# Kernel tuning notes

Hardware: AMD Instinct MI355X
Metric: run time of the kernel (lower is better)

The kernel has to match this reference:

```python
import jax, jax.numpy as jnp
import numpy as np

HEADS = 8
DIM_HEAD = 64
SCALE = DIM_HEAD ** -0.5


def setup_inputs() -> dict:
    key = jax.random.key(0)
    ks = jax.random.split(key, 5)
    dim, hidden = 512, HEADS * DIM_HEAD
    b, l = 4, 2048
    return {
        "x": jax.random.normal(ks[0], (b, dim, l), jnp.float32),
        "w_qkv": jax.random.normal(ks[1], (3 * hidden, dim), jnp.float32) * 0.02,
        "b_qkv": jax.random.normal(ks[2], (3 * hidden,), jnp.float32) * 0.02,
        "w_out": jax.random.normal(ks[3], (dim, hidden), jnp.float32) * 0.02,
        "b_out": jax.random.normal(ks[4], (dim,), jnp.float32) * 0.02,
    }


def reference(x, w_qkv, b_qkv, w_out, b_out):
    b, c, l = x.shape
    # Conv1d kernel-size-1 == per-position linear: (b, 3*hidden, l)
    qkv = jnp.einsum('oc,bcl->bol', w_qkv, x) + b_qkv[None, :, None]
    q, k, v = jnp.split(qkv, 3, axis=1)
    # rearrange 'b (h d) l -> b h d l'
    def split_heads(t):
        return t.reshape(b, HEADS, DIM_HEAD, l)
    q, k, v = split_heads(q) * SCALE, split_heads(k), split_heads(v)
    sim = jnp.einsum('bhdi,bhdj->bhij', q, k)  # [b,h,l,l]
    sim = sim - jax.lax.stop_gradient(jnp.max(sim, axis=-1, keepdims=True))
    attn = jax.nn.softmax(sim, axis=-1)
    out = jnp.einsum('bhij,bhdj->bhid', attn, v)  # [b,h,l,d]
    # 'b h l d -> b (h d) l'
    out = out.transpose(0, 1, 3, 2).reshape(b, HEADS * DIM_HEAD, l)
    out = jnp.einsum('oc,bcl->bol', w_out, out) + b_out[None, :, None]
    return out
```

## Files before the change

kernel.cpp:

```cpp
#include <hip/hip_runtime.h>
#include <hip/hip_bf16.h>

#define B 4
#define DIM 512
#define HID 512
#define NH 8
#define DH 64
#define L 2048
#define QSCALE (0.125f * 1.4426950408889634f)

typedef __attribute__((ext_vector_type(8)))  short bf16x8;
typedef __attribute__((ext_vector_type(4)))  float f32x4;
typedef __attribute__((ext_vector_type(16))) float f32x16;
typedef __attribute__((ext_vector_type(4)))  int   i32x4;

static __device__ __forceinline__ short f32_to_bf16s(float f) {
    __hip_bfloat16 h = __float2bfloat16(f);
    return *reinterpret_cast<short*>(&h);
}
static __device__ __forceinline__ float bf16s_to_f32(short s) {
    return __uint_as_float(((unsigned)(unsigned short)s) << 16);
}

static __device__ __forceinline__ float fast_exp2(float x) {
    float r;
    asm("v_exp_f32 %0, %1" : "=v"(r) : "v"(x));
    return r;
}

static __device__ __forceinline__ void gl_lds16(const short* g, short* l) {
    __builtin_amdgcn_global_load_lds(
        (const __attribute__((address_space(1))) void*)g,
        (__attribute__((address_space(3))) void*)l, 16, 0, 0);
}

static __device__ __forceinline__ bf16x8 lds_frag(const short* t, int row, int c) {
    bf16x8 v;
    __builtin_memcpy(&v, t + row * 64 + ((c ^ (row & 7)) * 8), 16);
    return v;
}

static __device__ __forceinline__ bf16x8 lds_vfrag(const short* t, int row,
                                                   int c0, int me4) {
    int2 a, b;
    __builtin_memcpy(&a, t + row * 64 + ((c0 ^ (row & 7)) * 8 + me4), 8);
    __builtin_memcpy(&b, t + row * 64 + (((c0 + 1) ^ (row & 7)) * 8 + me4), 8);
    i32x4 v = {a.x, a.y, b.x, b.y};
    return __builtin_bit_cast(bf16x8, v);
}

__global__ __launch_bounds__(256) void prep(
    const float* __restrict__ wq, const float* __restrict__ wo,
    short* __restrict__ wdst,
    const float* __restrict__ X, short* __restrict__ XT)
{
    const int bx  = blockIdx.x;
    const int tid = threadIdx.x;
    if (bx < 1024) {
        const int i = (bx * 256 + tid) * 4;
        float4 v;
        if (i < 786432) v = *(const float4*)(wq + i);
        else            v = *(const float4*)(wo + (i - 786432));
        short4 pk = {f32_to_bf16s(v.x), f32_to_bf16s(v.y),
                     f32_to_bf16s(v.z), f32_to_bf16s(v.w)};
        *(short4*)(wdst + i) = pk;
        return;
    }
    const int bid = bx - 1024;
    const int l0 = (bid & 31) * 64;
    const int c0 = ((bid >> 5) & 7) * 64;
    const int b  = bid >> 8;

    __shared__ float tile[64][65];
    const float* Xb = X + (size_t)b * DIM * L;

    #pragma unroll
    for (int it = 0; it < 16; ++it) {
        const int cr = (tid >> 6) + it * 4;
        const int lc = tid & 63;
        tile[cr][lc] = Xb[(size_t)(c0 + cr) * L + l0 + lc];
    }
    __syncthreads();
    short* XTb = XT + (size_t)b * L * DIM;
    #pragma unroll
    for (int it = 0; it < 8; ++it) {
        const int l  = (tid >> 5) + it * 8;
        const int c2 = (tid & 31) * 2;
        short2 pk = {f32_to_bf16s(tile[c2][l]), f32_to_bf16s(tile[c2 + 1][l])};
        *(short2*)(XTb + (size_t)(l0 + l) * DIM + c0 + c2) = pk;
    }
}

__global__ __launch_bounds__(256) void qkv_mfma(
    const short* __restrict__ Wb, const short* __restrict__ XT,
    const float* __restrict__ bias,
    short* __restrict__ qws, short* __restrict__ kws, short* __restrict__ vws)
{
    const int lBase = blockIdx.x * 128;
    const int oBase = blockIdx.y * 128;
    const int b     = blockIdx.z;
    const int tid   = threadIdx.x;
    const int wave  = tid >> 6;
    const int lane  = tid & 63;
    const int lid   = lane & 15;
    const int quad  = lane >> 4;
    const int rsub  = lane >> 3;
    const int cl    = (lane & 7) ^ rsub;

    __shared__ __align__(16) short Wt[128 * 64];
    __shared__ __align__(16) short Xt[128 * 64];

    const short* XTb = XT + (size_t)b * L * DIM;
    const int oLoc = (wave & 1) * 64;
    const int lLoc = (wave >> 1) * 64;

    f32x4 acc[4][4];
    #pragma unroll
    for (int mi = 0; mi < 4; ++mi)
        #pragma unroll
        for (int ni = 0; ni < 4; ++ni) acc[mi][ni] = (f32x4){0.f, 0.f, 0.f, 0.f};

    for (int c0 = 0; c0 < DIM; c0 += 64) {
        if (c0) __syncthreads();
        #pragma unroll
        for (int t = 0; t < 4; ++t) {
            const int ch = wave * 4 + t;
            const int r  = ch * 8 + rsub;
            gl_lds16(Wb  + (size_t)(oBase + r) * DIM + c0 + cl * 8, Wt + ch * 512);
            gl_lds16(XTb + (size_t)(lBase + r) * DIM + c0 + cl * 8, Xt + ch * 512);
        }
        __syncthreads();
        #pragma unroll
        for (int kc = 0; kc < 2; ++kc) {
            bf16x8 a[4], bb[4];
            #pragma unroll
            for (int mi = 0; mi < 4; ++mi)
                a[mi] = lds_frag(Wt, oLoc + mi * 16 + lid, kc * 4 + quad);
            #pragma unroll
            for (int ni = 0; ni < 4; ++ni)
                bb[ni] = lds_frag(Xt, lLoc + ni * 16 + lid, kc * 4 + quad);
            #pragma unroll
            for (int mi = 0; mi < 4; ++mi)
                #pragma unroll
                for (int ni = 0; ni < 4; ++ni)
                    acc[mi][ni] = __builtin_amdgcn_mfma_f32_16x16x32_bf16(
                        a[mi], bb[ni], acc[mi][ni], 0, 0, 0);
        }
    }

    const int rty = oBase >> 9;
    const float sc = (rty == 0) ? QSCALE : 1.0f;
    const int h = ((oBase + oLoc) >> 6) & 7;

    #pragma unroll
    for (int mi = 0; mi < 4; ++mi) {
        const int dB = mi * 16 + quad * 4;
        float bia[4];
        #pragma unroll
        for (int r = 0; r < 4; ++r)
            bia[r] = bias[oBase + oLoc + mi * 16 + quad * 4 + r];

        if (rty < 2) {
            short* dst = (rty == 0 ? qws : kws) + (((size_t)b * NH + h) * L) * DH;
            #pragma unroll
            for (int ni = 0; ni < 4; ++ni) {
                const int l = lBase + lLoc + ni * 16 + lid;
                short4 pk = {f32_to_bf16s((acc[mi][ni][0] + bia[0]) * sc),
                             f32_to_bf16s((acc[mi][ni][1] + bia[1]) * sc),
                             f32_to_bf16s((acc[mi][ni][2] + bia[2]) * sc),
                             f32_to_bf16s((acc[mi][ni][3] + bia[3]) * sc)};
                *(short4*)(dst + (size_t)l * DH + dB) = pk;
            }
        } else {
            short* dst = vws + (((size_t)b * NH + h) * DH) * L;
            #pragma unroll
            for (int r = 0; r < 4; ++r) {
                const int d = dB + r;
                #pragma unroll
                for (int ni = 0; ni < 4; ++ni)
                    dst[(size_t)d * L + lBase + lLoc + ni * 16 + lid] =
                        f32_to_bf16s((acc[mi][ni][r] + bia[r]) * sc);
            }
        }
    }
}

__global__ __launch_bounds__(256) void attn_mfma(
    const short* __restrict__ Q, const short* __restrict__ K,
    const short* __restrict__ VT,
    short* __restrict__ Op0, short* __restrict__ Op1,
    short* __restrict__ Op2, short* __restrict__ Op3,
    float* __restrict__ Lp)
{
    const int h     = blockIdx.x >> 2;
    const int qtr   = blockIdx.x & 3;
    const int b     = blockIdx.y;
    const int iTile = blockIdx.z;
    const int tid   = threadIdx.x;
    const int wave  = tid >> 6;
    const int lane  = tid & 63;
    const int l5    = lane & 31;
    const int me    = lane >> 5;
    const int me4   = me * 4;
    const int rsub  = lane >> 3;
    const int cl    = (lane & 7) ^ rsub;

    short* __restrict__ Op = (qtr & 2) ? ((qtr & 1) ? Op3 : Op2)
                                       : ((qtr & 1) ? Op1 : Op0);
    float* __restrict__ Lq = Lp + (size_t)qtr * (B * NH * L);

    const size_t headOff = ((size_t)b * NH + h) * (size_t)L * DH;
    const short* Qh = Q + headOff;
    const short* Kh = K + headOff;
    const short* Vh = VT + headOff;

    __shared__ __align__(16) short Kt[64 * 64];
    __shared__ __align__(16) short Vt[64 * 64];

    const int q0 = iTile * 128 + wave * 32;
    bf16x8 qf[4];
    #pragma unroll
    for (int kc = 0; kc < 4; ++kc)
        qf[kc] = *(const bf16x8*)(Qh + (size_t)(q0 + l5) * DH + kc * 16 + me4 * 2);

    const i32x4 onesI = {0x3F803F80, 0x3F803F80, 0x3F803F80, 0x3F803F80};
    const bf16x8 ones = __builtin_bit_cast(bf16x8, onesI);

    f32x16 oacc[2], lacc;
    #pragma unroll
    for (int dt = 0; dt < 2; ++dt)
        #pragma unroll
        for (int r = 0; r < 16; ++r) oacc[dt][r] = 0.f;
    #pragma unroll
    for (int r = 0; r < 16; ++r) lacc[r] = 0.f;

    const int jt0 = qtr * 8;
    for (int it = 0; it < 8; ++it) {
        const int j0 = (jt0 + it) * 64;
        if (it) __syncthreads();
        #pragma unroll
        for (int t = 0; t < 2; ++t) {
            const int ch = wave * 2 + t;
            const int r  = ch * 8 + rsub;
            gl_lds16(Kh + (size_t)(j0 + r) * DH + cl * 8, Kt + ch * 512);
            gl_lds16(Vh + (size_t)r * L + j0 + cl * 8,    Vt + ch * 512);
        }
        __syncthreads();

        unsigned dw[2][4][2];
        #pragma unroll
        for (int mt = 0; mt < 2; ++mt) {
            f32x16 s;
            #pragma unroll
            for (int r = 0; r < 16; ++r) s[r] = 0.f;
            #pragma unroll
            for (int kc = 0; kc < 4; ++kc) {
                bf16x8 a = lds_frag(Kt, mt * 32 + l5, kc * 2 + me);
                s = __builtin_amdgcn_mfma_f32_32x32x16_bf16(a, qf[kc], s, 0, 0, 0);
            }
            #pragma unroll
            for (int g = 0; g < 4; ++g) {
                #pragma unroll
                for (int p = 0; p < 2; ++p) {
                    const float p0 = fast_exp2(s[4 * g + 2 * p]);
                    const float p1 = fast_exp2(s[4 * g + 2 * p + 1]);
                    dw[mt][g][p] = __builtin_amdgcn_perm(
                        __float_as_uint(p1), __float_as_uint(p0), 0x07060302u);
                }
            }
        }

        #pragma unroll
        for (int mt = 0; mt < 2; ++mt) {
            #pragma unroll
            for (int kl = 0; kl < 2; ++kl) {
                i32x4 bi = {(int)dw[mt][2 * kl][0], (int)dw[mt][2 * kl][1],
                            (int)dw[mt][2 * kl + 1][0], (int)dw[mt][2 * kl + 1][1]};
                bf16x8 pb = __builtin_bit_cast(bf16x8, bi);
                lacc = __builtin_amdgcn_mfma_f32_32x32x16_bf16(ones, pb, lacc, 0, 0, 0);
                const int c0 = mt * 4 + kl * 2;
                #pragma unroll
                for (int dt = 0; dt < 2; ++dt) {
                    bf16x8 a = lds_vfrag(Vt, dt * 32 + l5, c0, me4);
                    oacc[dt] = __builtin_amdgcn_mfma_f32_32x32x16_bf16(a, pb, oacc[dt], 0, 0, 0);
                }
            }
        }
    }

    const float vh = lacc[0];
    const int qg = q0 + l5;
    if (me == 0)
        Lq[((size_t)b * NH + h) * L + qg] = vh;

    const float inv = 1.0f / vh;
    short* ab = Op + ((size_t)b * L + qg) * HID + h * DH;
    #pragma unroll
    for (int dt = 0; dt < 2; ++dt) {
        #pragma unroll
        for (int g = 0; g < 4; ++g) {
            const int d = dt * 32 + 8 * g + me4;
            short4 pk = {f32_to_bf16s(oacc[dt][4 * g]     * inv),
                         f32_to_bf16s(oacc[dt][4 * g + 1] * inv),
                         f32_to_bf16s(oacc[dt][4 * g + 2] * inv),
                         f32_to_bf16s(oacc[dt][4 * g + 3] * inv)};
            *(short4*)(ab + d) = pk;
        }
    }
}

__global__ __launch_bounds__(256) void combine4(
    const short* __restrict__ O0, const short* __restrict__ O1,
    const short* __restrict__ O2, const short* __restrict__ O3,
    const float* __restrict__ Lp, short* __restrict__ Abf)
{
    const int g = blockIdx.x * 256 + threadIdx.x;
    const int i = g * 4;
    const int b = i >> 20;
    const int rem = i & 1048575;
    const int l = rem >> 9;
    const int c = rem & 511;
    const int h = c >> 6;
    const size_t li = ((size_t)b * NH + h) * L + l;
    const float w0 = Lp[li];
    const float w1 = Lp[li + (size_t)B * NH * L];
    const float w2 = Lp[li + (size_t)2 * B * NH * L];
    const float w3 = Lp[li + (size_t)3 * B * NH * L];
    const float inv = 1.0f / (w0 + w1 + w2 + w3);
    const short4 a = *(const short4*)(O0 + i);
    const short4 bb = *(const short4*)(O1 + i);
    const short4 cc = *(const short4*)(O2 + i);
    const short4 dd = *(const short4*)(O3 + i);
    short4 pk = {
        f32_to_bf16s((w0 * bf16s_to_f32(a.x) + w1 * bf16s_to_f32(bb.x) +
                      w2 * bf16s_to_f32(cc.x) + w3 * bf16s_to_f32(dd.x)) * inv),
        f32_to_bf16s((w0 * bf16s_to_f32(a.y) + w1 * bf16s_to_f32(bb.y) +
                      w2 * bf16s_to_f32(cc.y) + w3 * bf16s_to_f32(dd.y)) * inv),
        f32_to_bf16s((w0 * bf16s_to_f32(a.z) + w1 * bf16s_to_f32(bb.z) +
                      w2 * bf16s_to_f32(cc.z) + w3 * bf16s_to_f32(dd.z)) * inv),
        f32_to_bf16s((w0 * bf16s_to_f32(a.w) + w1 * bf16s_to_f32(bb.w) +
                      w2 * bf16s_to_f32(cc.w) + w3 * bf16s_to_f32(dd.w)) * inv)};
    *(short4*)(Abf + i) = pk;
}

__global__ __launch_bounds__(256) void out_mfma(
    const short* __restrict__ Wo, const short* __restrict__ Abf,
    const float* __restrict__ bias, float* __restrict__ out)
{
    const int lBase = blockIdx.x * 128;
    const int oBase = blockIdx.y * 64;
    const int b     = blockIdx.z;
    const int tid   = threadIdx.x;
    const int wave  = tid >> 6;
    const int lane  = tid & 63;
    const int lid   = lane & 15;
    const int quad  = lane >> 4;
    const int rsub  = lane >> 3;
    const int cl    = (lane & 7) ^ rsub;

    __shared__ __align__(16) short Wt[64 * 64];
    __shared__ __align__(16) short At[128 * 64];

    const short* Ab = Abf + (size_t)b * L * HID;
    const int oLoc = (wave & 1) * 32;
    const int lLoc = (wave >> 1) * 64;

    f32x4 acc[2][4];
    #pragma unroll
    for (int mi = 0; mi < 2; ++mi)
        #pragma unroll
        for (int ni = 0; ni < 4; ++ni) acc[mi][ni] = (f32x4){0.f, 0.f, 0.f, 0.f};

    for (int c0 = 0; c0 < HID; c0 += 64) {
        if (c0) __syncthreads();
        #pragma unroll
        for (int t = 0; t < 2; ++t) {
            const int ch = wave * 2 + t;
            const int r  = ch * 8 + rsub;
            gl_lds16(Wo + (size_t)(oBase + r) * HID + c0 + cl * 8, Wt + ch * 512);
        }
        #pragma unroll
        for (int t = 0; t < 4; ++t) {
            const int ch = wave * 4 + t;
            const int r  = ch * 8 + rsub;
            gl_lds16(Ab + (size_t)(lBase + r) * HID + c0 + cl * 8, At + ch * 512);
        }
        __syncthreads();
        #pragma unroll
        for (int kc = 0; kc < 2; ++kc) {
            bf16x8 a[2], bb[4];
            #pragma unroll
            for (int mi = 0; mi < 2; ++mi)
                a[mi] = lds_frag(Wt, oLoc + mi * 16 + lid, kc * 4 + quad);
            #pragma unroll
            for (int ni = 0; ni < 4; ++ni)
                bb[ni] = lds_frag(At, lLoc + ni * 16 + lid, kc * 4 + quad);
            #pragma unroll
            for (int mi = 0; mi < 2; ++mi)
                #pragma unroll
                for (int ni = 0; ni < 4; ++ni)
                    acc[mi][ni] = __builtin_amdgcn_mfma_f32_16x16x32_bf16(
                        a[mi], bb[ni], acc[mi][ni], 0, 0, 0);
        }
    }

    #pragma unroll
    for (int mi = 0; mi < 2; ++mi) {
        #pragma unroll
        for (int r = 0; r < 4; ++r) {
            const int o = oBase + oLoc + mi * 16 + quad * 4 + r;
            const float bia = bias[o];
            #pragma unroll
            for (int ni = 0; ni < 4; ++ni)
                out[((size_t)b * DIM + o) * L + lBase + lLoc + ni * 16 + lid] =
                    acc[mi][ni][r] + bia;
        }
    }
}

extern "C" void kernel_launch(void* const* d_in, const int* in_sizes, int n_in,
                              void* d_out, int out_size, void* d_ws, size_t ws_size,
                              hipStream_t stream)
{
    const float* x     = (const float*)d_in[0];
    const float* w_qkv = (const float*)d_in[1];
    const float* b_qkv = (const float*)d_in[2];
    const float* w_out = (const float*)d_in[3];
    const float* b_out = (const float*)d_in[4];
    float* out = (float*)d_out;

    char* w = (char*)d_ws;
    short* xT  = (short*)(w);
    short* wqb = (short*)(w + (8u << 20));
    short* wob = wqb + 786432;
    short* qws = (short*)(w + (10u << 20));
    short* kws = (short*)(w + (18u << 20));
    short* vws = (short*)(w + (26u << 20));
    short* Abf = (short*)(w + (34u << 20));
    short* Op1 = (short*)(w);
    short* Op2 = (short*)(w + (42u << 20));
    short* Op3 = (short*)(w + (50u << 20));
    float* Lp  = (float*)(w + (58u << 20));
    short* Op0 = (short*)d_out;

    dim3 blk(256);
    prep<<<dim3(2048), blk, 0, stream>>>(w_qkv, w_out, wqb, x, xT);
    qkv_mfma<<<dim3(L / 128, 1536 / 128, B), blk, 0, stream>>>(
        wqb, xT, b_qkv, qws, kws, vws);
    attn_mfma<<<dim3(NH * 4, B, L / 128), blk, 0, stream>>>(
        qws, kws, vws, Op0, Op1, Op2, Op3, Lp);
    combine4<<<dim3(4096), blk, 0, stream>>>(Op0, Op1, Op2, Op3, Lp, Abf);
    out_mfma<<<dim3(L / 128, DIM / 64, B), blk, 0, stream>>>(
        wob, Abf, b_out, out);
}
```

Before: 170.0 us.

## Permute V layout for 16-byte LDS reads and replace row-sum MFMA with VALU

The QKV projection now writes V^T with a lane permutation within each 16-column group. This lets the attention kernel fetch V fragments with a single 16-byte LDS read instead of two 8-byte reads, and the Q fragment load offset changes to keep the k-index ordering consistent. The softmax denominator is now accumulated with scalar VALU adds plus one cross-half shuffle, replacing the extra ones-vector MFMA per P block. This trades MFMA work for VALU adds and depends on the permutation being matched exactly between producer and consumer.

```diff
diff --git a/kernel.cpp b/kernel.cpp
--- a/kernel.cpp
+++ b/kernel.cpp
@@ -38,15 +38,6 @@
     bf16x8 v;
     __builtin_memcpy(&v, t + row * 64 + ((c ^ (row & 7)) * 8), 16);
     return v;
-}
-
-static __device__ __forceinline__ bf16x8 lds_vfrag(const short* t, int row,
-                                                   int c0, int me4) {
-    int2 a, b;
-    __builtin_memcpy(&a, t + row * 64 + ((c0 ^ (row & 7)) * 8 + me4), 8);
-    __builtin_memcpy(&b, t + row * 64 + (((c0 + 1) ^ (row & 7)) * 8 + me4), 8);
-    i32x4 v = {a.x, a.y, b.x, b.y};
-    return __builtin_bit_cast(bf16x8, v);
 }
 
 __global__ __launch_bounds__(256) void prep(
@@ -151,6 +142,7 @@
     const int rty = oBase >> 9;
     const float sc = (rty == 0) ? QSCALE : 1.0f;
     const int h = ((oBase + oLoc) >> 6) & 7;
+    const int pl = (lid & 3) | ((lid & 4) << 1) | ((lid & 8) >> 1);
 
     #pragma unroll
     for (int mi = 0; mi < 4; ++mi) {
@@ -178,7 +170,7 @@
                 const int d = dB + r;
                 #pragma unroll
                 for (int ni = 0; ni < 4; ++ni)
-                    dst[(size_t)d * L + lBase + lLoc + ni * 16 + lid] =
+                    dst[(size_t)d * L + lBase + lLoc + ni * 16 + pl] =
                         f32_to_bf16s((acc[mi][ni][r] + bia[r]) * sc);
             }
         }
@@ -201,7 +193,6 @@
     const int lane  = tid & 63;
     const int l5    = lane & 31;
     const int me    = lane >> 5;
-    const int me4   = me * 4;
     const int rsub  = lane >> 3;
     const int cl    = (lane & 7) ^ rsub;
 
@@ -221,18 +212,14 @@
     bf16x8 qf[4];
     #pragma unroll
     for (int kc = 0; kc < 4; ++kc)
-        qf[kc] = *(const bf16x8*)(Qh + (size_t)(q0 + l5) * DH + kc * 16 + me4 * 2);
-
-    const i32x4 onesI = {0x3F803F80, 0x3F803F80, 0x3F803F80, 0x3F803F80};
-    const bf16x8 ones = __builtin_bit_cast(bf16x8, onesI);
-
-    f32x16 oacc[2], lacc;
+        qf[kc] = *(const bf16x8*)(Qh + (size_t)(q0 + l5) * DH + kc * 16 + me * 8);
+
+    f32x16 oacc[2];
     #pragma unroll
     for (int dt = 0; dt < 2; ++dt)
         #pragma unroll
         for (int r = 0; r < 16; ++r) oacc[dt][r] = 0.f;
-    #pragma unroll
-    for (int r = 0; r < 16; ++r) lacc[r] = 0.f;
+    float lsum = 0.f;
 
     const int jt0 = qtr * 8;
     for (int it = 0; it < 8; ++it) {
@@ -264,8 +251,11 @@
                 for (int p = 0; p < 2; ++p) {
                     const float p0 = fast_exp2(s[4 * g + 2 * p]);
                     const float p1 = fast_exp2(s[4 * g + 2 * p + 1]);
-                    dw[mt][g][p] = __builtin_amdgcn_perm(
+                    const unsigned pk = __builtin_amdgcn_perm(
                         __float_as_uint(p1), __float_as_uint(p0), 0x07060302u);
+                    lsum += __uint_as_float(pk << 16);
+                    lsum += __uint_as_float(pk & 0xffff0000u);
+                    dw[mt][g][p] = pk;
                 }
             }
         }
@@ -277,18 +267,17 @@
                 i32x4 bi = {(int)dw[mt][2 * kl][0], (int)dw[mt][2 * kl][1],
                             (int)dw[mt][2 * kl + 1][0], (int)dw[mt][2 * kl + 1][1]};
                 bf16x8 pb = __builtin_bit_cast(bf16x8, bi);
-                lacc = __builtin_amdgcn_mfma_f32_32x32x16_bf16(ones, pb, lacc, 0, 0, 0);
-                const int c0 = mt * 4 + kl * 2;
+                const int ch = (mt * 2 + kl) * 2 + me;
                 #pragma unroll
                 for (int dt = 0; dt < 2; ++dt) {
-                    bf16x8 a = lds_vfrag(Vt, dt * 32 + l5, c0, me4);
+                    bf16x8 a = lds_frag(Vt, dt * 32 + l5, ch);
                     oacc[dt] = __builtin_amdgcn_mfma_f32_32x32x16_bf16(a, pb, oacc[dt], 0, 0, 0);
                 }
             }
         }
     }
 
-    const float vh = lacc[0];
+    const float vh = lsum + __shfl_xor(lsum, 32);
     const int qg = q0 + l5;
     if (me == 0)
         Lq[((size_t)b * NH + h) * L + qg] = vh;
@@ -299,7 +288,7 @@
     for (int dt = 0; dt < 2; ++dt) {
         #pragma unroll
         for (int g = 0; g < 4; ++g) {
-            const int d = dt * 32 + 8 * g + me4;
+            const int d = dt * 32 + 8 * g + me * 4;
             short4 pk = {f32_to_bf16s(oacc[dt][4 * g]     * inv),
                          f32_to_bf16s(oacc[dt][4 * g + 1] * inv),
                          f32_to_bf16s(oacc[dt][4 * g + 2] * inv),
```

Result: faster. 161.9 us (-4.8%).
